# Kernel optimization log

Hardware: AMD Instinct MI355X
Metric: run time of the kernel (lower is better)

Reference implementation:

```python
import jax, jax.numpy as jnp
import numpy as np

N_QUBITS = 7
N_LAYERS = 4
DIM = 2 ** N_QUBITS  # 128


def _cnot_perm(c, t, n=N_QUBITS):
    # PennyLane convention: wire 0 is the most-significant bit of the state index.
    idx = np.arange(2 ** n)
    ctrl = (idx >> (n - 1 - c)) & 1
    flipped = idx ^ (1 << (n - 1 - t))
    return np.where(ctrl == 1, flipped, idx)

# StronglyEntanglingLayers with a single layer uses range r=1: CNOT(j, (j+1) % n)
CNOT_PERMS = tuple(jnp.asarray(_cnot_perm(j, (j + 1) % N_QUBITS)) for j in range(N_QUBITS))

_bits = (np.arange(DIM)[None, :] >> (N_QUBITS - 1 - np.arange(N_QUBITS)[:, None])) & 1
Z_SIGNS = jnp.asarray(1.0 - 2.0 * _bits, dtype=jnp.float32)  # (7,128): +1 if wire bit 0 else -1


def _apply_1q(state, U, q):
    # state: (B,128) complex; U: (B,2,2) batched or (2,2) shared
    B = state.shape[0]
    s = state.reshape(B, 2 ** q, 2, 2 ** (N_QUBITS - 1 - q))
    if U.ndim == 3:
        s = jnp.einsum('bij,bpjq->bpiq', U, s)
    else:
        s = jnp.einsum('ij,bpjq->bpiq', U, s)
    return s.reshape(B, DIM)


def _simulate(x, weights):
    # x: (B,7) angles; weights: (4,7,3) Rot params. Returns <Z_q> per wire: (B,7)
    B = x.shape[0]
    state = jnp.zeros((B, DIM), jnp.complex64).at[:, 0].set(1.0)
    half = 0.5 * x
    c = jnp.cos(half).astype(jnp.complex64)  # (B,7)
    s = jnp.sin(half).astype(jnp.complex64)
    for l in range(N_LAYERS):
        # AngleEmbedding: RX(x_j) on wire j (data re-uploading, same x each block)
        for q in range(N_QUBITS):
            cq, sq = c[:, q], s[:, q]
            U = jnp.stack([jnp.stack([cq, -1j * sq], axis=-1),
                           jnp.stack([-1j * sq, cq], axis=-1)], axis=-2)  # (B,2,2)
            state = _apply_1q(state, U, q)
        # StronglyEntanglingLayers single layer: Rot(phi,theta,omega) per wire
        for q in range(N_QUBITS):
            phi, theta, omega = weights[l, q, 0], weights[l, q, 1], weights[l, q, 2]
            ct = jnp.cos(0.5 * theta).astype(jnp.complex64)
            st = jnp.sin(0.5 * theta).astype(jnp.complex64)
            ep = jnp.exp(-0.5j * (phi + omega).astype(jnp.complex64))
            em = jnp.exp(-0.5j * (phi - omega).astype(jnp.complex64))
            # Rot = RZ(omega) @ RY(theta) @ RZ(phi)
            U = jnp.stack([jnp.stack([ep * ct, -jnp.conj(em) * st]),
                           jnp.stack([em * st, jnp.conj(ep) * ct])])  # (2,2)
            state = _apply_1q(state, U, q)
        # entangler: CNOT(j, j+1 mod 7) for all j
        for q in range(N_QUBITS):
            state = state[:, CNOT_PERMS[q]]
    probs = state.real ** 2 + state.imag ** 2  # (B,128)
    return probs @ Z_SIGNS.T  # (B,7)


def setup_inputs() -> dict:
    key = jax.random.key(0)
    ks = jax.random.split(key, 6)
    B, n_classes = 16384, 22
    return {
        'x': jax.random.uniform(ks[0], (B, N_QUBITS), jnp.float32),
        'weights': jax.random.normal(ks[1], (N_LAYERS, N_QUBITS, 3), jnp.float32),
        'fc1_w': jax.random.normal(ks[2], (32, N_QUBITS), jnp.float32) * 0.3,
        'fc1_b': jax.random.normal(ks[3], (32,), jnp.float32) * 0.1,
        'fc2_w': jax.random.normal(ks[4], (n_classes, 32), jnp.float32) * 0.2,
        'fc2_b': jax.random.normal(ks[5], (n_classes,), jnp.float32) * 0.1,
    }


def reference(x, weights, fc1_w, fc1_b, fc2_w, fc2_b):
    q_out = _simulate(x, weights)                      # (B,7)
    h = jax.nn.relu(q_out @ fc1_w.T + fc1_b)           # (B,32); dropout is inference no-op
    return h @ fc2_w.T + fc2_b                         # (B,n_classes)
```

## Files before the change

### kernel.cpp

```cpp
#include <hip/hip_runtime.h>

constexpr int NQ = 7;
constexpr int NL = 4;
constexpr int NG = NL * NQ;
constexpr int NCLS = 22;
constexpr int EPB = 16;

typedef float v2 __attribute__((ext_vector_type(2)));
#define FMA2(a,b,c) __builtin_elementwise_fma((a),(b),(c))

__device__ __forceinline__ v2 sp(float s) { v2 r; r.x = s; r.y = s; return r; }
__device__ __forceinline__ v2 mkv2(float a, float b) { v2 r; r.x = a; r.y = b; return r; }
__device__ __forceinline__ v2 sel(bool c, v2 a, v2 b) {
    v2 r; r.x = c ? a.x : b.x; r.y = c ? a.y : b.y; return r;
}

template<int CTRL>
__device__ __forceinline__ float fdpp(float v) {
    return __int_as_float(__builtin_amdgcn_mov_dpp(__float_as_int(v), CTRL, 0xF, 0xF, true));
}
template<int OFF>
__device__ __forceinline__ float fswz(float v) {
    return __int_as_float(__builtin_amdgcn_ds_swizzle(__float_as_int(v), OFF));
}
template<int M>
__device__ __forceinline__ float xorl(float v) {
    if      constexpr (M == 1)  return fdpp<0xB1>(v);
    else if constexpr (M == 2)  return fdpp<0x4E>(v);
    else if constexpr (M == 4)  return fswz<0x101F>(v);
    else                        return fdpp<0x128>(v);
}
template<int M>
__device__ __forceinline__ v2 shufv(v2 v) {
    v2 r; r.x = xorl<M>(v.x); r.y = xorl<M>(v.y); return r;
}

__device__ __forceinline__ void fuse(const float* __restrict__ u, float c, float s,
                                     float4& A, float4& B) {
    A.x = fmaf(c, u[0],  s * u[3]);  A.y = fmaf(c, u[1], -s * u[2]);
    A.z = fmaf(c, u[2],  s * u[1]);  A.w = fmaf(c, u[3], -s * u[0]);
    B.x = fmaf(c, u[4],  s * u[7]);  B.y = fmaf(c, u[5], -s * u[6]);
    B.z = fmaf(c, u[6],  s * u[5]);  B.w = fmaf(c, u[7], -s * u[4]);
}

template<int M>
__device__ __forceinline__ void gateLane(int lane, float4 A, float4 B,
                                         v2 X[4], v2 Y[4]) {
    const bool hi = (lane & M) != 0;
    const float cvr = hi ? B.z : A.x, cvi = hi ? B.w : A.y;
    const float cwr = hi ? B.x : A.z, cwi = hi ? B.y : A.w;
    v2 Xs[4], Ys[4];
    #pragma unroll
    for (int j = 0; j < 4; ++j) { Xs[j] = shufv<M>(X[j]); Ys[j] = shufv<M>(Y[j]); }
    #pragma unroll
    for (int j = 0; j < 4; ++j) {
        v2 nX = FMA2(sp(cvr), X[j], FMA2(sp(-cvi), Y[j], FMA2(sp(cwr), Xs[j], sp(-cwi)*Ys[j])));
        v2 nY = FMA2(sp(cvr), Y[j], FMA2(sp( cvi), X[j], FMA2(sp(cwr), Ys[j], sp( cwi)*Xs[j])));
        X[j] = nX; Y[j] = nY;
    }
}

__device__ __forceinline__ void gateCross(float4 A, float4 B,
                                          v2& Xa, v2& Ya, v2& Xb, v2& Yb) {
    v2 nXa = FMA2(sp(A.x), Xa, FMA2(sp(-A.y), Ya, FMA2(sp(A.z), Xb, sp(-A.w)*Yb)));
    v2 nYa = FMA2(sp(A.x), Ya, FMA2(sp( A.y), Xa, FMA2(sp(A.z), Yb, sp( A.w)*Xb)));
    v2 nXb = FMA2(sp(B.x), Xa, FMA2(sp(-B.y), Ya, FMA2(sp(B.z), Xb, sp(-B.w)*Yb)));
    v2 nYb = FMA2(sp(B.x), Ya, FMA2(sp( B.y), Xa, FMA2(sp(B.z), Yb, sp( B.w)*Xb)));
    Xa = nXa; Ya = nYa; Xb = nXb; Yb = nYb;
}

__global__ __launch_bounds__(256) void reupload_kernel(
    const float* __restrict__ x,
    const float* __restrict__ wts,
    const float* __restrict__ fc1_w,
    const float* __restrict__ fc1_b,
    const float* __restrict__ fc2_w,
    const float* __restrict__ fc2_b,
    float* __restrict__ out,
    int B)
{
    __shared__ __align__(16) float rotU[NG * 8];
    __shared__ float2 csb[EPB * NQ];
    __shared__ __align__(16) float fU[NG * EPB * 8];
    __shared__ __align__(16) float fUT[NL * EPB * 8];
    __shared__ __align__(16) float hbuf[EPB][32];

    const int tid = threadIdx.x;
    if (tid < EPB * NQ) {
        const int e = tid / NQ, q = tid % NQ;
        const int bb = blockIdx.x * EPB + e;
        const float xv = (bb < B) ? x[bb*NQ + q] : 0.f;
        const float h = 0.5f * xv;
        csb[tid] = make_float2(__cosf(h), __sinf(h));
    } else if (tid >= 128 && tid < 128 + NG) {
        const int g = tid - 128;
        float phi = wts[g*3+0], th = wts[g*3+1], om = wts[g*3+2];
        float ct = __cosf(0.5f*th), st = __sinf(0.5f*th);
        float ap = 0.5f*(phi+om),  am = 0.5f*(phi-om);
        float cp = __cosf(ap), sp_ = __sinf(ap);
        float cm = __cosf(am), sm = __sinf(am);
        float* u = &rotU[g*8];
        u[0] =  cp*ct; u[1] = -sp_*ct;
        u[2] = -cm*st; u[3] = -sm*st;
        u[4] =  cm*st; u[5] = -sm*st;
        u[6] =  cp*ct; u[7] =  sp_*ct;
    }
    __syncthreads();
    #pragma unroll
    for (int i = tid; i < NG * EPB; i += 256) {
        const int g = i >> 4, e = i & 15;
        const int q = g % NQ;
        const float2 cs = csb[e*NQ + q];
        float4 A, Bq;
        fuse(&rotU[g*8], cs.x, cs.y, A, Bq);
        float4* dst = reinterpret_cast<float4*>(&fU[(g*EPB + e)*8]);
        dst[0] = A; dst[1] = Bq;
        if (q == 5) {
            const int l = g / NQ;
            float* td = &fUT[(l*EPB + e)*8];
            td[0] = A.x; td[1] = Bq.x; td[2] = A.y; td[3] = Bq.y;
            td[4] = A.z; td[5] = Bq.z; td[6] = A.w; td[7] = Bq.w;
        }
    }
    __syncthreads();

    const int lane = threadIdx.x & 63;
    const int u    = threadIdx.x & 15;
    const int grp  = threadIdx.x >> 4;
    const int b    = blockIdx.x * EPB + grp;
    if (b >= B) return;

    const int srcLane = (lane & 48) | ((u ^ (u >> 1)) & 15);

    v2 X[4], Y[4];
    #pragma unroll
    for (int j = 0; j < 4; ++j) { X[j] = sp(0.f); Y[j] = sp(0.f); }
    X[0].x = (u == 0) ? 1.f : 0.f;

    #pragma unroll
    for (int l = 0; l < NL; ++l) {
        float4 A, Bq;
        #define LOADU(q) { const float4* up = reinterpret_cast<const float4*>( \
            &fU[((l*NQ + (q))*EPB + grp)*8]); A = up[0]; Bq = up[1]; }
        LOADU(0); gateLane<8>(lane, A, Bq, X, Y);
        LOADU(1); gateLane<4>(lane, A, Bq, X, Y);
        LOADU(2); gateLane<2>(lane, A, Bq, X, Y);
        LOADU(3); gateLane<1>(lane, A, Bq, X, Y);
        LOADU(4);
        gateCross(A, Bq, X[0], Y[0], X[2], Y[2]);
        gateCross(A, Bq, X[1], Y[1], X[3], Y[3]);
        {
            const v2* tp = reinterpret_cast<const v2*>(&fUT[(l*EPB + grp)*8]);
            const v2 c00r = tp[0], c00i = tp[1], c01r = tp[2], c01i = tp[3];
            #pragma unroll
            for (int j = 0; j < 4; ++j) {
                const v2 Xxx = X[j].xx, Xyy = X[j].yy;
                const v2 Yxx = Y[j].xx, Yyy = Y[j].yy;
                v2 nX = FMA2(c00r, Xxx, FMA2(-c00i, Yxx, FMA2(c01r, Xyy, (-c01i)*Yyy)));
                v2 nY = FMA2(c00r, Yxx, FMA2( c00i, Xxx, FMA2(c01r, Yyy, ( c01i)*Xyy)));
                X[j] = nX; Y[j] = nY;
            }
        }
        LOADU(6);
        gateCross(A, Bq, X[0], Y[0], X[1], Y[1]);
        gateCross(A, Bq, X[2], Y[2], X[3], Y[3]);
        #undef LOADU

        #pragma unroll
        for (int j = 0; j < 4; ++j) {
            X[j].x = __shfl(X[j].x, srcLane); X[j].y = __shfl(X[j].y, srcLane);
            Y[j].x = __shfl(Y[j].x, srcLane); Y[j].y = __shfl(Y[j].y, srcLane);
        }
        {
            const bool cc = (lane & 1) != 0;
            v2 t;
            t = X[0]; X[0] = sel(cc, X[2], X[0]); X[2] = sel(cc, t, X[2]);
            t = X[1]; X[1] = sel(cc, X[3], X[1]); X[3] = sel(cc, t, X[3]);
            t = Y[0]; Y[0] = sel(cc, Y[2], Y[0]); Y[2] = sel(cc, t, Y[2]);
            t = Y[1]; Y[1] = sel(cc, Y[3], Y[1]); Y[3] = sel(cc, t, Y[3]);
        }
        {
            X[2] = X[2].yx; X[3] = X[3].yx; Y[2] = Y[2].yx; Y[3] = Y[3].yx;
        }
        {
            float t;
            t = X[0].y; X[0].y = X[1].y; X[1].y = t;
            t = X[2].y; X[2].y = X[3].y; X[3].y = t;
            t = Y[0].y; Y[0].y = Y[1].y; Y[1].y = t;
            t = Y[2].y; Y[2].y = Y[3].y; Y[3].y = t;
        }
        {
            X[1] = shufv<8>(X[1]); X[3] = shufv<8>(X[3]);
            Y[1] = shufv<8>(Y[1]); Y[3] = shufv<8>(Y[3]);
        }
    }

    v2 P[4];
    #pragma unroll
    for (int j = 0; j < 4; ++j) P[j] = FMA2(X[j], X[j], Y[j]*Y[j]);
    const v2 Sa = P[0] + P[1], Sb = P[2] + P[3];
    const v2 Se = P[0] + P[2], So = P[1] + P[3];
    const v2 T  = Sa + Sb;
    const float t = T.x + T.y;
    v2 zv[3];
    zv[0] = mkv2((lane & 8) ? -t : t, (lane & 4) ? -t : t);
    zv[1] = mkv2((lane & 2) ? -t : t, (lane & 1) ? -t : t);
    zv[2] = mkv2((Sa.x + Sa.y) - (Sb.x + Sb.y),
                 T.x - T.y);
    float z6 = (Se.x + Se.y) - (So.x + So.y);
    #pragma unroll
    for (int j = 0; j < 3; ++j) {
        v2 v = zv[j];
        v2 s1; s1.x = xorl<1>(v.x); s1.y = xorl<1>(v.y); v += s1;
        v2 s2; s2.x = xorl<2>(v.x); s2.y = xorl<2>(v.y); v += s2;
        v2 q4;  q4.x  = fdpp<0x124>(v.x); q4.y  = fdpp<0x124>(v.y);
        v2 q8;  q8.x  = fdpp<0x128>(v.x); q8.y  = fdpp<0x128>(v.y);
        v2 q12; q12.x = fdpp<0x12C>(v.x); q12.y = fdpp<0x12C>(v.y);
        zv[j] = (v + q8) + (q4 + q12);
    }
    {
        float v = z6;
        v += xorl<1>(v);
        v += xorl<2>(v);
        const float q4 = fdpp<0x124>(v), q8 = fdpp<0x128>(v), q12 = fdpp<0x12C>(v);
        z6 = (v + q8) + (q4 + q12);
    }

    const float* wra = fc1_w + u*NQ;
    const float* wrb = fc1_w + (u+16)*NQ;
    v2 da = FMA2(zv[0], mkv2(wra[0], wra[1]),
            FMA2(zv[1], mkv2(wra[2], wra[3]),
                 zv[2] * mkv2(wra[4], wra[5])));
    v2 db = FMA2(zv[0], mkv2(wrb[0], wrb[1]),
            FMA2(zv[1], mkv2(wrb[2], wrb[3]),
                 zv[2] * mkv2(wrb[4], wrb[5])));
    const float acc1a = fc1_b[u]      + da.x + da.y + z6 * wra[6];
    const float acc1b = fc1_b[u + 16] + db.x + db.y + z6 * wrb[6];
    hbuf[grp][u]      = fmaxf(acc1a, 0.f);
    hbuf[grp][u + 16] = fmaxf(acc1b, 0.f);
    __builtin_amdgcn_wave_barrier();
    asm volatile("s_waitcnt lgkmcnt(0)" ::: "memory");
    __builtin_amdgcn_sched_barrier(0);

    v2 hv[16];
    #pragma unroll
    for (int i = 0; i < 8; ++i) {
        float4 v4 = *reinterpret_cast<const float4*>(&hbuf[grp][i*4]);
        hv[2*i]   = mkv2(v4.x, v4.y);
        hv[2*i+1] = mkv2(v4.z, v4.w);
    }
    const int kb = (u < NCLS - 16) ? (u + 16) : 0;
    const float4* w4a = reinterpret_cast<const float4*>(fc2_w + u*32);
    const float4* w4b = reinterpret_cast<const float4*>(fc2_w + kb*32);
    v2 a2 = sp(0.f), b2 = sp(0.f);
    #pragma unroll
    for (int i = 0; i < 8; ++i) {
        float4 wa = w4a[i], wb = w4b[i];
        a2 = FMA2(hv[2*i],   mkv2(wa.x, wa.y), a2);
        a2 = FMA2(hv[2*i+1], mkv2(wa.z, wa.w), a2);
        b2 = FMA2(hv[2*i],   mkv2(wb.x, wb.y), b2);
        b2 = FMA2(hv[2*i+1], mkv2(wb.z, wb.w), b2);
    }
    const float acc2a = fc2_b[u]  + a2.x + a2.y;
    const float acc2b = fc2_b[kb] + b2.x + b2.y;
    out[b*NCLS + u] = acc2a;
    if (u < NCLS - 16) out[b*NCLS + 16 + u] = acc2b;
}

extern "C" void kernel_launch(void* const* d_in, const int* in_sizes, int n_in,
                              void* d_out, int out_size, void* d_ws, size_t ws_size,
                              hipStream_t stream) {
    const float* x     = (const float*)d_in[0];
    const float* wts   = (const float*)d_in[1];
    const float* fc1_w = (const float*)d_in[2];
    const float* fc1_b = (const float*)d_in[3];
    const float* fc2_w = (const float*)d_in[4];
    const float* fc2_b = (const float*)d_in[5];
    float* out = (float*)d_out;

    const int B = in_sizes[0] / NQ;
    const int grid = (B + EPB - 1) / EPB;
    reupload_kernel<<<grid, 256, 0, stream>>>(x, wts, fc1_w, fc1_b, fc2_w, fc2_b, out, B);
}
```

Measured before the change: 20.11 us.

## Process two batch elements per thread group to raise ILP and amortize setup

Each block now handles 32 batch elements instead of 16, and each 16-lane group simulates two independent state vectors interleaved through every gate, CNOT shuffle, reduction and FC stage. The interleaving is meant to hide shuffle, DPP and LDS latency with independent work. It also spreads the per-block setup (gate fusion, syncs) over more elements and halves the grid. In exchange, register pressure roughly doubles and there are half as many resident waves, which could reduce occupancy on the CUs.

```diff
diff --git a/kernel.cpp b/kernel.cpp
--- a/kernel.cpp
+++ b/kernel.cpp
@@ -4,7 +4,7 @@
 constexpr int NL = 4;
 constexpr int NG = NL * NQ;
 constexpr int NCLS = 22;
-constexpr int EPB = 16;
+constexpr int EPB = 32;
 
 typedef float v2 __attribute__((ext_vector_type(2)));
 #define FMA2(a,b,c) __builtin_elementwise_fma((a),(b),(c))
@@ -67,6 +67,44 @@
     v2 nXb = FMA2(sp(B.x), Xa, FMA2(sp(-B.y), Ya, FMA2(sp(B.z), Xb, sp(-B.w)*Yb)));
     v2 nYb = FMA2(sp(B.x), Ya, FMA2(sp( B.y), Xa, FMA2(sp(B.z), Yb, sp( B.w)*Xb)));
     Xa = nXa; Ya = nYa; Xb = nXb; Yb = nYb;
+}
+
+__device__ __forceinline__ void gateComp(const v2* __restrict__ tp, v2 X[4], v2 Y[4]) {
+    const v2 c00r = tp[0], c00i = tp[1], c01r = tp[2], c01i = tp[3];
+    #pragma unroll
+    for (int j = 0; j < 4; ++j) {
+        const v2 Xxx = X[j].xx, Xyy = X[j].yy;
+        const v2 Yxx = Y[j].xx, Yyy = Y[j].yy;
+        v2 nX = FMA2(c00r, Xxx, FMA2(-c00i, Yxx, FMA2(c01r, Xyy, (-c01i)*Yyy)));
+        v2 nY = FMA2(c00r, Yxx, FMA2( c00i, Xxx, FMA2(c01r, Yyy, ( c01i)*Xyy)));
+        X[j] = nX; Y[j] = nY;
+    }
+}
+
+__device__ __forceinline__ void cnotTail(int lane, int srcLane, v2 X[4], v2 Y[4]) {
+    #pragma unroll
+    for (int j = 0; j < 4; ++j) {
+        X[j].x = __shfl(X[j].x, srcLane); X[j].y = __shfl(X[j].y, srcLane);
+        Y[j].x = __shfl(Y[j].x, srcLane); Y[j].y = __shfl(Y[j].y, srcLane);
+    }
+    {
+        const bool cc = (lane & 1) != 0;
+        v2 t;
+        t = X[0]; X[0] = sel(cc, X[2], X[0]); X[2] = sel(cc, t, X[2]);
+        t = X[1]; X[1] = sel(cc, X[3], X[1]); X[3] = sel(cc, t, X[3]);
+        t = Y[0]; Y[0] = sel(cc, Y[2], Y[0]); Y[2] = sel(cc, t, Y[2]);
+        t = Y[1]; Y[1] = sel(cc, Y[3], Y[1]); Y[3] = sel(cc, t, Y[3]);
+    }
+    X[2] = X[2].yx; X[3] = X[3].yx; Y[2] = Y[2].yx; Y[3] = Y[3].yx;
+    {
+        float t;
+        t = X[0].y; X[0].y = X[1].y; X[1].y = t;
+        t = X[2].y; X[2].y = X[3].y; X[3].y = t;
+        t = Y[0].y; Y[0].y = Y[1].y; Y[1].y = t;
+        t = Y[2].y; Y[2].y = Y[3].y; Y[3].y = t;
+    }
+    X[1] = shufv<8>(X[1]); X[3] = shufv<8>(X[3]);
+    Y[1] = shufv<8>(Y[1]); Y[3] = shufv<8>(Y[3]);
 }
 
 __global__ __launch_bounds__(256) void reupload_kernel(
@@ -92,8 +130,8 @@
         const float xv = (bb < B) ? x[bb*NQ + q] : 0.f;
         const float h = 0.5f * xv;
         csb[tid] = make_float2(__cosf(h), __sinf(h));
-    } else if (tid >= 128 && tid < 128 + NG) {
-        const int g = tid - 128;
+    } else if (tid >= 224 && tid < 224 + NG) {
+        const int g = tid - 224;
         float phi = wts[g*3+0], th = wts[g*3+1], om = wts[g*3+2];
         float ct = __cosf(0.5f*th), st = __sinf(0.5f*th);
         float ap = 0.5f*(phi+om),  am = 0.5f*(phi-om);
@@ -108,7 +146,7 @@
     __syncthreads();
     #pragma unroll
     for (int i = tid; i < NG * EPB; i += 256) {
-        const int g = i >> 4, e = i & 15;
+        const int g = i >> 5, e = i & 31;
         const int q = g % NQ;
         const float2 cs = csb[e*NQ + q];
         float4 A, Bq;
@@ -127,144 +165,150 @@
     const int lane = threadIdx.x & 63;
     const int u    = threadIdx.x & 15;
     const int grp  = threadIdx.x >> 4;
-    const int b    = blockIdx.x * EPB + grp;
-    if (b >= B) return;
+    const int b0   = blockIdx.x * EPB + grp;
+    const int b1   = b0 + 16;
+    if (b0 >= B) return;
 
     const int srcLane = (lane & 48) | ((u ^ (u >> 1)) & 15);
 
-    v2 X[4], Y[4];
-    #pragma unroll
-    for (int j = 0; j < 4; ++j) { X[j] = sp(0.f); Y[j] = sp(0.f); }
-    X[0].x = (u == 0) ? 1.f : 0.f;
+    v2 X0[4], Y0[4], X1[4], Y1[4];
+    #pragma unroll
+    for (int j = 0; j < 4; ++j) {
+        X0[j] = sp(0.f); Y0[j] = sp(0.f);
+        X1[j] = sp(0.f); Y1[j] = sp(0.f);
+    }
+    X0[0].x = (u == 0) ? 1.f : 0.f;
+    X1[0].x = (u == 0) ? 1.f : 0.f;
 
     #pragma unroll
     for (int l = 0; l < NL; ++l) {
-        float4 A, Bq;
-        #define LOADU(q) { const float4* up = reinterpret_cast<const float4*>( \
-            &fU[((l*NQ + (q))*EPB + grp)*8]); A = up[0]; Bq = up[1]; }
-        LOADU(0); gateLane<8>(lane, A, Bq, X, Y);
-        LOADU(1); gateLane<4>(lane, A, Bq, X, Y);
-        LOADU(2); gateLane<2>(lane, A, Bq, X, Y);
-        LOADU(3); gateLane<1>(lane, A, Bq, X, Y);
-        LOADU(4);
-        gateCross(A, Bq, X[0], Y[0], X[2], Y[2]);
-        gateCross(A, Bq, X[1], Y[1], X[3], Y[3]);
-        {
-            const v2* tp = reinterpret_cast<const v2*>(&fUT[(l*EPB + grp)*8]);
-            const v2 c00r = tp[0], c00i = tp[1], c01r = tp[2], c01i = tp[3];
-            #pragma unroll
-            for (int j = 0; j < 4; ++j) {
-                const v2 Xxx = X[j].xx, Xyy = X[j].yy;
-                const v2 Yxx = Y[j].xx, Yyy = Y[j].yy;
-                v2 nX = FMA2(c00r, Xxx, FMA2(-c00i, Yxx, FMA2(c01r, Xyy, (-c01i)*Yyy)));
-                v2 nY = FMA2(c00r, Yxx, FMA2( c00i, Xxx, FMA2(c01r, Yyy, ( c01i)*Xyy)));
-                X[j] = nX; Y[j] = nY;
-            }
-        }
-        LOADU(6);
-        gateCross(A, Bq, X[0], Y[0], X[1], Y[1]);
-        gateCross(A, Bq, X[2], Y[2], X[3], Y[3]);
-        #undef LOADU
-
+        float4 A0, B0, A1, B1;
+        #define LOADU2(q) { \
+            const float4* p0 = reinterpret_cast<const float4*>(&fU[((l*NQ + (q))*EPB + grp)*8]); \
+            A0 = p0[0]; B0 = p0[1]; \
+            const float4* p1 = reinterpret_cast<const float4*>(&fU[((l*NQ + (q))*EPB + grp + 16)*8]); \
+            A1 = p1[0]; B1 = p1[1]; }
+        LOADU2(0); gateLane<8>(lane, A0, B0, X0, Y0); gateLane<8>(lane, A1, B1, X1, Y1);
+        LOADU2(1); gateLane<4>(lane, A0, B0, X0, Y0); gateLane<4>(lane, A1, B1, X1, Y1);
+        LOADU2(2); gateLane<2>(lane, A0, B0, X0, Y0); gateLane<2>(lane, A1, B1, X1, Y1);
+        LOADU2(3); gateLane<1>(lane, A0, B0, X0, Y0); gateLane<1>(lane, A1, B1, X1, Y1);
+        LOADU2(4);
+        gateCross(A0, B0, X0[0], Y0[0], X0[2], Y0[2]);
+        gateCross(A0, B0, X0[1], Y0[1], X0[3], Y0[3]);
+        gateCross(A1, B1, X1[0], Y1[0], X1[2], Y1[2]);
+        gateCross(A1, B1, X1[1], Y1[1], X1[3], Y1[3]);
+        gateComp(reinterpret_cast<const v2*>(&fUT[(l*EPB + grp)*8]),      X0, Y0);
+        gateComp(reinterpret_cast<const v2*>(&fUT[(l*EPB + grp + 16)*8]), X1, Y1);
+        LOADU2(6);
+        gateCross(A0, B0, X0[0], Y0[0], X0[1], Y0[1]);
+        gateCross(A0, B0, X0[2], Y0[2], X0[3], Y0[3]);
+        gateCross(A1, B1, X1[0], Y1[0], X1[1], Y1[1]);
+        gateCross(A1, B1, X1[2], Y1[2], X1[3], Y1[3]);
+        #undef LOADU2
+
+        cnotTail(lane, srcLane, X0, Y0);
+        cnotTail(lane, srcLane, X1, Y1);
+    }
+
+    v2 zv0[3], zv1[3]; float z6_0, z6_1;
+    {
+        v2 P[4];
         #pragma unroll
-        for (int j = 0; j < 4; ++j) {
-            X[j].x = __shfl(X[j].x, srcLane); X[j].y = __shfl(X[j].y, srcLane);
-            Y[j].x = __shfl(Y[j].x, srcLane); Y[j].y = __shfl(Y[j].y, srcLane);
-        }
-        {
-            const bool cc = (lane & 1) != 0;
-            v2 t;
-            t = X[0]; X[0] = sel(cc, X[2], X[0]); X[2] = sel(cc, t, X[2]);
-            t = X[1]; X[1] = sel(cc, X[3], X[1]); X[3] = sel(cc, t, X[3]);
-            t = Y[0]; Y[0] = sel(cc, Y[2], Y[0]); Y[2] = sel(cc, t, Y[2]);
-            t = Y[1]; Y[1] = sel(cc, Y[3], Y[1]); Y[3] = sel(cc, t, Y[3]);
-        }
-        {
-            X[2] = X[2].yx; X[3] = X[3].yx; Y[2] = Y[2].yx; Y[3] = Y[3].yx;
-        }
-        {
-            float t;
-            t = X[0].y; X[0].y = X[1].y; X[1].y = t;
-            t = X[2].y; X[2].y = X[3].y; X[3].y = t;
-            t = Y[0].y; Y[0].y = Y[1].y; Y[1].y = t;
-            t = Y[2].y; Y[2].y = Y[3].y; Y[3].y = t;
-        }
-        {
-            X[1] = shufv<8>(X[1]); X[3] = shufv<8>(X[3]);
-            Y[1] = shufv<8>(Y[1]); Y[3] = shufv<8>(Y[3]);
-        }
-    }
-
-    v2 P[4];
-    #pragma unroll
-    for (int j = 0; j < 4; ++j) P[j] = FMA2(X[j], X[j], Y[j]*Y[j]);
-    const v2 Sa = P[0] + P[1], Sb = P[2] + P[3];
-    const v2 Se = P[0] + P[2], So = P[1] + P[3];
-    const v2 T  = Sa + Sb;
-    const float t = T.x + T.y;
-    v2 zv[3];
-    zv[0] = mkv2((lane & 8) ? -t : t, (lane & 4) ? -t : t);
-    zv[1] = mkv2((lane & 2) ? -t : t, (lane & 1) ? -t : t);
-    zv[2] = mkv2((Sa.x + Sa.y) - (Sb.x + Sb.y),
-                 T.x - T.y);
-    float z6 = (Se.x + Se.y) - (So.x + So.y);
+        for (int j = 0; j < 4; ++j) P[j] = FMA2(X0[j], X0[j], Y0[j]*Y0[j]);
+        const v2 Sa = P[0] + P[1], Sb = P[2] + P[3];
+        const v2 Se = P[0] + P[2], So = P[1] + P[3];
+        const v2 T  = Sa + Sb;
+        const float t = T.x + T.y;
+        zv0[0] = mkv2((lane & 8) ? -t : t, (lane & 4) ? -t : t);
+        zv0[1] = mkv2((lane & 2) ? -t : t, (lane & 1) ? -t : t);
+        zv0[2] = mkv2((Sa.x + Sa.y) - (Sb.x + Sb.y), T.x - T.y);
+        z6_0 = (Se.x + Se.y) - (So.x + So.y);
+    }
+    {
+        v2 P[4];
+        #pragma unroll
+        for (int j = 0; j < 4; ++j) P[j] = FMA2(X1[j], X1[j], Y1[j]*Y1[j]);
+        const v2 Sa = P[0] + P[1], Sb = P[2] + P[3];
+        const v2 Se = P[0] + P[2], So = P[1] + P[3];
+        const v2 T  = Sa + Sb;
+        const float t = T.x + T.y;
+        zv1[0] = mkv2((lane & 8) ? -t : t, (lane & 4) ? -t : t);
+        zv1[1] = mkv2((lane & 2) ? -t : t, (lane & 1) ? -t : t);
+        zv1[2] = mkv2((Sa.x + Sa.y) - (Sb.x + Sb.y), T.x - T.y);
+        z6_1 = (Se.x + Se.y) - (So.x + So.y);
+    }
     #pragma unroll
     for (int j = 0; j < 3; ++j) {
-        v2 v = zv[j];
+        v2 v = zv0[j];
         v2 s1; s1.x = xorl<1>(v.x); s1.y = xorl<1>(v.y); v += s1;
         v2 s2; s2.x = xorl<2>(v.x); s2.y = xorl<2>(v.y); v += s2;
         v2 q4;  q4.x  = fdpp<0x124>(v.x); q4.y  = fdpp<0x124>(v.y);
         v2 q8;  q8.x  = fdpp<0x128>(v.x); q8.y  = fdpp<0x128>(v.y);
         v2 q12; q12.x = fdpp<0x12C>(v.x); q12.y = fdpp<0x12C>(v.y);
-        zv[j] = (v + q8) + (q4 + q12);
-    }
-    {
-        float v = z6;
-        v += xorl<1>(v);
-        v += xorl<2>(v);
+        zv0[j] = (v + q8) + (q4 + q12);
+        v2 w = zv1[j];
+        v2 t1; t1.x = xorl<1>(w.x); t1.y = xorl<1>(w.y); w += t1;
+        v2 t2; t2.x = xorl<2>(w.x); t2.y = xorl<2>(w.y); w += t2;
+        v2 r4;  r4.x  = fdpp<0x124>(w.x); r4.y  = fdpp<0x124>(w.y);
+        v2 r8;  r8.x  = fdpp<0x128>(w.x); r8.y  = fdpp<0x128>(w.y);
+        v2 r12; r12.x = fdpp<0x12C>(w.x); r12.y = fdpp<0x12C>(w.y);
+        zv1[j] = (w + r8) + (r4 + r12);
+    }
+    {
+        float v = z6_0;
+        v += xorl<1>(v); v += xorl<2>(v);
         const float q4 = fdpp<0x124>(v), q8 = fdpp<0x128>(v), q12 = fdpp<0x12C>(v);
-        z6 = (v + q8) + (q4 + q12);
+        z6_0 = (v + q8) + (q4 + q12);
+        float w = z6_1;
+        w += xorl<1>(w); w += xorl<2>(w);
+        const float r4 = fdpp<0x124>(w), r8 = fdpp<0x128>(w), r12 = fdpp<0x12C>(w);
+        z6_1 = (w + r8) + (r4 + r12);
     }
 
     const float* wra = fc1_w + u*NQ;
     const float* wrb = fc1_w + (u+16)*NQ;
-    v2 da = FMA2(zv[0], mkv2(wra[0], wra[1]),
-            FMA2(zv[1], mkv2(wra[2], wra[3]),
-                 zv[2] * mkv2(wra[4], wra[5])));
-    v2 db = FMA2(zv[0], mkv2(wrb[0], wrb[1]),
-            FMA2(zv[1], mkv2(wrb[2], wrb[3]),
-                 zv[2] * mkv2(wrb[4], wrb[5])));
-    const float acc1a = fc1_b[u]      + da.x + da.y + z6 * wra[6];
-    const float acc1b = fc1_b[u + 16] + db.x + db.y + z6 * wrb[6];
-    hbuf[grp][u]      = fmaxf(acc1a, 0.f);
-    hbuf[grp][u + 16] = fmaxf(acc1b, 0.f);
+    {
+        v2 da = FMA2(zv0[0], mkv2(wra[0], wra[1]),
+                FMA2(zv0[1], mkv2(wra[2], wra[3]), zv0[2] * mkv2(wra[4], wra[5])));
+        v2 db = FMA2(zv0[0], mkv2(wrb[0], wrb[1]),
+                FMA2(zv0[1], mkv2(wrb[2], wrb[3]), zv0[2] * mkv2(wrb[4], wrb[5])));
+        hbuf[grp][u]      = fmaxf(fc1_b[u]      + da.x + da.y + z6_0 * wra[6], 0.f);
+        hbuf[grp][u + 16] = fmaxf(fc1_b[u + 16] + db.x + db.y + z6_0 * wrb[6], 0.f);
+        v2 dc = FMA2(zv1[0], mkv2(wra[0], wra[1]),
+                FMA2(zv1[1], mkv2(wra[2], wra[3]), zv1[2] * mkv2(wra[4], wra[5])));
+        v2 dd = FMA2(zv1[0], mkv2(wrb[0], wrb[1]),
+                FMA2(zv1[1], mkv2(wrb[2], wrb[3]), zv1[2] * mkv2(wrb[4], wrb[5])));
+        hbuf[grp + 16][u]      = fmaxf(fc1_b[u]      + dc.x + dc.y + z6_1 * wra[6], 0.f);
+        hbuf[grp + 16][u + 16] = fmaxf(fc1_b[u + 16] + dd.x + dd.y + z6_1 * wrb[6], 0.f);
+    }
     __builtin_amdgcn_wave_barrier();
     asm volatile("s_waitcnt lgkmcnt(0)" ::: "memory");
     __builtin_amdgcn_sched_barrier(0);
 
-    v2 hv[16];
-    #pragma unroll
-    for (int i = 0; i < 8; ++i) {
-        float4 v4 = *reinterpret_cast<const float4*>(&hbuf[grp][i*4]);
-        hv[2*i]   = mkv2(v4.x, v4.y);
-        hv[2*i+1] = mkv2(v4.z, v4.w);
-    }
     const int kb = (u < NCLS - 16) ? (u + 16) : 0;
     const float4* w4a = reinterpret_cast<const float4*>(fc2_w + u*32);
     const float4* w4b = reinterpret_cast<const float4*>(fc2_w + kb*32);
-    v2 a2 = sp(0.f), b2 = sp(0.f);
+    v2 a0 = sp(0.f), b0v = sp(0.f), a1 = sp(0.f), b1v = sp(0.f);
     #pragma unroll
     for (int i = 0; i < 8; ++i) {
+        float4 h0 = *reinterpret_cast<const float4*>(&hbuf[grp][i*4]);
+        float4 h1 = *reinterpret_cast<const float4*>(&hbuf[grp + 16][i*4]);
         float4 wa = w4a[i], wb = w4b[i];
-        a2 = FMA2(hv[2*i],   mkv2(wa.x, wa.y), a2);
-        a2 = FMA2(hv[2*i+1], mkv2(wa.z, wa.w), a2);
-        b2 = FMA2(hv[2*i],   mkv2(wb.x, wb.y), b2);
-        b2 = FMA2(hv[2*i+1], mkv2(wb.z, wb.w), b2);
-    }
-    const float acc2a = fc2_b[u]  + a2.x + a2.y;
-    const float acc2b = fc2_b[kb] + b2.x + b2.y;
-    out[b*NCLS + u] = acc2a;
-    if (u < NCLS - 16) out[b*NCLS + 16 + u] = acc2b;
+        a0  = FMA2(mkv2(h0.x, h0.y), mkv2(wa.x, wa.y), a0);
+        a0  = FMA2(mkv2(h0.z, h0.w), mkv2(wa.z, wa.w), a0);
+        b0v = FMA2(mkv2(h0.x, h0.y), mkv2(wb.x, wb.y), b0v);
+        b0v = FMA2(mkv2(h0.z, h0.w), mkv2(wb.z, wb.w), b0v);
+        a1  = FMA2(mkv2(h1.x, h1.y), mkv2(wa.x, wa.y), a1);
+        a1  = FMA2(mkv2(h1.z, h1.w), mkv2(wa.z, wa.w), a1);
+        b1v = FMA2(mkv2(h1.x, h1.y), mkv2(wb.x, wb.y), b1v);
+        b1v = FMA2(mkv2(h1.z, h1.w), mkv2(wb.z, wb.w), b1v);
+    }
+    out[b0*NCLS + u] = fc2_b[u] + a0.x + a0.y;
+    if (u < NCLS - 16) out[b0*NCLS + 16 + u] = fc2_b[kb] + b0v.x + b0v.y;
+    if (b1 < B) {
+        out[b1*NCLS + u] = fc2_b[u] + a1.x + a1.y;
+        if (u < NCLS - 16) out[b1*NCLS + 16 + u] = fc2_b[kb] + b1v.x + b1v.y;
+    }
 }
 
 extern "C" void kernel_launch(void* const* d_in, const int* in_sizes, int n_in,
```

Measured after the change: 21.48 us. 1.07x slower.
